# Performance work log

Measured on AMD Instinct MI355X. Metric: run time of the kernel, lower is better.

Reference implementation:

```python
import jax, jax.numpy as jnp
import numpy as np

B, T, N = 256, 512, 256
START, STOP = 254, 255


def setup_inputs() -> dict:
    key = jax.random.key(0)
    k1, k2, k3 = jax.random.split(key, 3)
    inputs = jax.random.normal(k1, (B, T, N), dtype=jnp.float32)
    transitions = jax.random.normal(k2, (N, N), dtype=jnp.float32)
    # sentinel rows/cols as in __init__
    transitions = transitions.at[START, :].set(-10000.0).at[:, STOP].set(-10000.0)
    tags = jax.random.randint(k3, (B, T), 0, N, dtype=jnp.int32)
    mask = jnp.ones((B, T), dtype=jnp.int32)
    return {"inputs": inputs, "transitions": transitions, "tags": tags, "mask": mask}


def _input_likelihood(inputs, transitions, fmask):
    # alpha[b, tag]: log-sum over paths ending at tag
    alpha0 = transitions[:, START][None, :] + inputs[:, 0, :]

    def step(alpha, xs):
        emit, m = xs  # emit: (B, N), m: (B,)
        # inner[b, next, prev] = alpha[b, prev] + (emit[b, next] + trans[next, prev]) * mask[b, i-1]
        inner = alpha[:, None, :] + (emit[:, :, None] + transitions[None, :, :]) * m[:, None, None]
        return jax.nn.logsumexp(inner, axis=-1), None

    xs = (jnp.swapaxes(inputs[:, 1:, :], 0, 1), jnp.swapaxes(fmask[:, :-1], 0, 1))
    alpha, _ = jax.lax.scan(step, alpha0, xs)
    stops = alpha + transitions[STOP][None, :]
    return jax.nn.logsumexp(stops, axis=-1)  # (B,)


def _joint_likelihood(inputs, transitions, tags, fmask):
    score = transitions[tags[:, 0], START]  # (B,)
    # transitions[next, prev] * mask[:, i+1], summed over steps
    trans_sc = transitions[tags[:, 1:], tags[:, :-1]] * fmask[:, 1:]
    # inputs[b, i, prev_tag] * mask[:, i]
    emit_sc = jnp.take_along_axis(inputs[:, :-1, :], tags[:, :-1, None], axis=2)[..., 0] * fmask[:, :-1]
    score = score + trans_sc.sum(axis=-1) + emit_sc.sum(axis=-1)
    last_idx = (fmask.sum(axis=-1) - 1.0).astype(jnp.int32)  # (B,)
    last_tags = jnp.take_along_axis(tags, last_idx[:, None], axis=1)[:, 0]
    last_input = jnp.take_along_axis(inputs[:, -1, :], last_tags[:, None], axis=1)[:, 0]
    return score + transitions[STOP, last_tags] + last_input * fmask[:, -1]


def reference(inputs, transitions, tags, mask):
    fmask = mask.astype(jnp.float32)
    log_denominator = _input_likelihood(inputs, transitions, fmask)
    log_numerator = _joint_likelihood(inputs, transitions, tags, fmask)
    return jnp.sum(log_numerator - log_denominator)
```

## Files before the change

kernel.cpp:

```cpp
#include <hip/hip_runtime.h>
#include <hip/hip_bf16.h>
#include <stdint.h>

#define B_    256
#define T_    512
#define N_    256
#define START_ 254
#define STOP_  255
#define GCOLS 16
#define NF    16
#define ND    32
#define LOG2E 1.4426950408889634f
#define LN2   0.6931471805599453f

#define WSB_OFF 65536
#define WCF_OFF 131072
#define WCB_OFF 131328

typedef __attribute__((ext_vector_type(4))) float floatx4;
typedef __attribute__((ext_vector_type(2))) long long llx2;
typedef __attribute__((ext_vector_type(4))) unsigned int uintx4;

__device__ __forceinline__ void lds_barrier() {
    asm volatile("s_waitcnt lgkmcnt(0)\n\ts_barrier" ::: "memory");
}

__device__ __forceinline__ int pk_fp8x4(float a, float b, float c, float d) {
    int r = __builtin_amdgcn_cvt_pk_fp8_f32(a, b, 0, false);
    return __builtin_amdgcn_cvt_pk_fp8_f32(c, d, r, true);
}
__device__ __forceinline__ int pk_bf8x4(float a, float b, float c, float d) {
    int r = __builtin_amdgcn_cvt_pk_bf8_f32(a, b, 0, false);
    return __builtin_amdgcn_cvt_pk_bf8_f32(c, d, r, true);
}
__device__ __forceinline__ long long mk64(int lo, int hi) {
    return ((long long)(unsigned long long)(unsigned)hi << 32) | (unsigned)lo;
}
__device__ __forceinline__ unsigned umax_(unsigned a, unsigned b) { return a > b ? a : b; }

struct DenomShared {
    alignas(16) char  V[2][4096];
    alignas(16) unsigned short mexp[GCOLS * 8];
    alignas(16) float sbuf[GCOLS * 20];
};

template<bool ISF>
__device__ __forceinline__ void denom_path(
    DenomShared& sh, const float* __restrict__ inputs,
    const float* __restrict__ trans, const int* __restrict__ mask,
    float* __restrict__ ws, int blkLocal)
{
    const int tid = threadIdx.x;
    const int w = tid >> 6;
    const int l = tid & 63;
    const int q = l >> 4;
    const int b = l & 15;
    const int bg = blkLocal * GCOLS + b;
    const int j0 = 32 * w + 4 * q;
    const int S = ISF ? 256 : 255;

    auto EIDX = [](int s) { return ISF ? s : (511 - s); };
    auto MIDX = [](int s) { return ISF ? (s - 1) : (511 - s); };

    const int wa0 = ((w >> 1) << 10) + ((q >> 1) << 8) + (b << 4)
                  + ((w & 1) << 3) + ((q & 1) << 2);
    const int rbase = l << 4;

    long long afrag[2][8];
    #pragma unroll
    for (int mt = 0; mt < 2; ++mt) {
        const int row = 32 * w + 16 * mt + b;
        #pragma unroll
        for (int kt = 0; kt < 8; ++kt) {
            float e[8];
            if (ISF) {
                const float* p = trans + row * N_ + kt * 32 + q * 8;
                floatx4 t0 = *(const floatx4*)p;
                floatx4 t1 = *(const floatx4*)(p + 4);
                #pragma unroll
                for (int jj = 0; jj < 4; ++jj) {
                    e[jj]     = __builtin_amdgcn_exp2f(t0[jj] * LOG2E);
                    e[jj + 4] = __builtin_amdgcn_exp2f(t1[jj] * LOG2E);
                }
            } else {
                #pragma unroll
                for (int jj = 0; jj < 8; ++jj) {
                    const int k = kt * 32 + q * 8 + jj;
                    e[jj] = __builtin_amdgcn_exp2f(trans[k * N_ + row] * LOG2E);
                }
            }
            afrag[mt][kt] = mk64(pk_fp8x4(e[0], e[1], e[2], e[3]),
                                 pk_fp8x4(e[4], e[5], e[6], e[7]));
        }
    }

    const float* emitp = inputs + (size_t)bg * T_ * N_;
    const int*   maskp = mask + bg * T_;
    float C = 0.f;
    float u[2][4];

    auto produce = [&]() {
        float mx = u[0][0], sm = 0.f;
        #pragma unroll
        for (int mt = 0; mt < 2; ++mt)
            #pragma unroll
            for (int r = 0; r < 4; ++r) { mx = fmaxf(mx, u[mt][r]); sm += u[mt][r]; }
        mx = fmaxf(mx, __shfl_xor(mx, 16, 64));
        mx = fmaxf(mx, __shfl_xor(mx, 32, 64));
        sm += __shfl_xor(sm, 32, 64);
        if (l < 16)
            sh.mexp[b * 8 + w] =
                (unsigned short)(__builtin_bit_cast(uint32_t, mx) >> 23);
        if (l < 32) sh.sbuf[b * 20 + w * 2 + q] = sm;
    };

    if (ISF) {
        #pragma unroll
        for (int mt = 0; mt < 2; ++mt) {
            floatx4 em = *(const floatx4*)(emitp + j0 + 16 * mt);
            #pragma unroll
            for (int r = 0; r < 4; ++r) {
                const int j = j0 + 16 * mt + r;
                u[mt][r] = __builtin_amdgcn_exp2f((trans[j * N_ + START_] + em[r]) * LOG2E);
            }
        }
    } else {
        #pragma unroll
        for (int mt = 0; mt < 2; ++mt) {
            floatx4 st = *(const floatx4*)(trans + STOP_ * N_ + j0 + 16 * mt);
            #pragma unroll
            for (int r = 0; r < 4; ++r)
                u[mt][r] = __builtin_amdgcn_exp2f(st[r] * LOG2E);
        }
    }
    {
        float xpi[2][4] = {{1.f,1.f,1.f,1.f},{1.f,1.f,1.f,1.f}};
        if (!ISF) {
            #pragma unroll
            for (int mt = 0; mt < 2; ++mt) {
                floatx4 e = *(const floatx4*)(emitp + (size_t)511 * N_ + j0 + 16 * mt);
                #pragma unroll
                for (int r = 0; r < 4; ++r)
                    xpi[mt][r] = __builtin_amdgcn_exp2f(e[r] * LOG2E);
            }
        }
        produce();
        #pragma unroll
        for (int mt = 0; mt < 2; ++mt)
            *(int*)(sh.V[0] + wa0 + (mt << 9)) =
                pk_bf8x4(u[mt][0] * xpi[mt][0], u[mt][1] * xpi[mt][1],
                         u[mt][2] * xpi[mt][2], u[mt][3] * xpi[mt][3]);
    }
    floatx4 ebuf[2][2];
    float   mrot[2];
    ebuf[0][0] = *(const floatx4*)(emitp + (size_t)EIDX(1) * N_ + j0);
    ebuf[0][1] = *(const floatx4*)(emitp + (size_t)EIDX(1) * N_ + j0 + 16);
    ebuf[1][0] = *(const floatx4*)(emitp + (size_t)EIDX(2) * N_ + j0);
    ebuf[1][1] = *(const floatx4*)(emitp + (size_t)EIDX(2) * N_ + j0 + 16);
    mrot[0] = (float)maskp[MIDX(1)];
    mrot[1] = (float)maskp[MIDX(2)];
    lds_barrier();

    auto body = [&](int s, int pr, int cur) {
        const int sp = (s + 2 <= S) ? s + 2 : S;
        floatx4 eC0 = *(const floatx4*)(emitp + (size_t)EIDX(sp) * N_ + j0);
        floatx4 eC1 = *(const floatx4*)(emitp + (size_t)EIDX(sp) * N_ + j0 + 16);
        const float mC = (float)maskp[MIDX(sp)];

        const char* vb = sh.V[pr];
        long long bf[8];
        #pragma unroll
        for (int p = 0; p < 4; ++p) {
            llx2 rd = *(const llx2*)(vb + (p << 10) + rbase);
            bf[2 * p]     = rd[0];
            bf[2 * p + 1] = rd[1];
        }

        uintx4 me = *(const uintx4*)&sh.mexp[b * 8];
        unsigned hi = umax_(umax_(me[0], me[1]), umax_(me[2], me[3]));
        unsigned lo = umax_(umax_(me[0] << 16, me[1] << 16),
                            umax_(me[2] << 16, me[3] << 16));
        const int eb = (int)(umax_(hi, lo) >> 16);
        const float rs = __builtin_bit_cast(float, (uint32_t)(249 - eb) << 23);
        const float dCf = (float)(122 - eb);

        float xpv[2][4];
        #pragma unroll
        for (int r = 0; r < 4; ++r) {
            if (ISF) {
                xpv[0][r] = __builtin_amdgcn_exp2f(fmaf(ebuf[cur][0][r], LOG2E, dCf));
                xpv[1][r] = __builtin_amdgcn_exp2f(fmaf(ebuf[cur][1][r], LOG2E, dCf));
            } else {
                xpv[0][r] = __builtin_amdgcn_exp2f(ebuf[cur][0][r] * LOG2E);
                xpv[1][r] = __builtin_amdgcn_exp2f(ebuf[cur][1][r] * LOG2E);
            }
        }

        floatx4 a0 = {0.f,0.f,0.f,0.f}, a1 = {0.f,0.f,0.f,0.f};
        floatx4 a2 = {0.f,0.f,0.f,0.f}, a3 = {0.f,0.f,0.f,0.f};
        #pragma unroll
        for (int kt = 0; kt < 4; ++kt) {
            a0 = __builtin_amdgcn_mfma_f32_16x16x32_fp8_bf8(afrag[0][kt],     bf[kt],     a0, 0, 0, 0);
            a1 = __builtin_amdgcn_mfma_f32_16x16x32_fp8_bf8(afrag[0][kt + 4], bf[kt + 4], a1, 0, 0, 0);
            a2 = __builtin_amdgcn_mfma_f32_16x16x32_fp8_bf8(afrag[1][kt],     bf[kt],     a2, 0, 0, 0);
            a3 = __builtin_amdgcn_mfma_f32_16x16x32_fp8_bf8(afrag[1][kt + 4], bf[kt + 4], a3, 0, 0, 0);
        }

        const bool live = (mrot[cur] != 0.f);
        float csv = 0.f;
        if (__any(!live)) {
            const float* sb = &sh.sbuf[b * 20];
            floatx4 s0 = *(const floatx4*)sb,       s1 = *(const floatx4*)(sb + 4);
            floatx4 s2 = *(const floatx4*)(sb + 8), s3 = *(const floatx4*)(sb + 12);
            csv = ((((s0[0] + s0[1]) + (s0[2] + s0[3])) +
                    ((s1[0] + s1[1]) + (s1[2] + s1[3]))) +
                   (((s2[0] + s2[1]) + (s2[2] + s2[3])) +
                    ((s3[0] + s3[1]) + (s3[2] + s3[3])))) * rs;
        }
        #pragma unroll
        for (int r = 0; r < 4; ++r) {
            const float v0 = a0[r] + a1[r], v1 = a2[r] + a3[r];
            if (ISF) {
                u[0][r] = live ? v0 * xpv[0][r] : csv;
                u[1][r] = live ? v1 * xpv[1][r] : csv;
            } else {
                u[0][r] = live ? v0 * rs : csv;
                u[1][r] = live ? v1 * rs : csv;
            }
        }
        C += (float)(eb - 122);

        produce();
        #pragma unroll
        for (int mt = 0; mt < 2; ++mt) {
            *(int*)(sh.V[pr ^ 1] + wa0 + (mt << 9)) = ISF
                ? pk_bf8x4(u[mt][0], u[mt][1], u[mt][2], u[mt][3])
                : pk_bf8x4(u[mt][0] * xpv[mt][0], u[mt][1] * xpv[mt][1],
                           u[mt][2] * xpv[mt][2], u[mt][3] * xpv[mt][3]);
        }
        lds_barrier();
        ebuf[cur][0] = eC0; ebuf[cur][1] = eC1;
        mrot[cur] = mC;
    };

    #pragma unroll 1
    for (int g = 0; g < 127; ++g) {
        body(2 * g + 1, 0, 0);
        body(2 * g + 2, 1, 1);
    }
    if (ISF) { body(255, 0, 0); body(256, 1, 1); }
    else     { body(255, 0, 0); }

    float* wsV = ws + (ISF ? 0 : WSB_OFF);
    #pragma unroll
    for (int mt = 0; mt < 2; ++mt) {
        floatx4 vv = {u[mt][0], u[mt][1], u[mt][2], u[mt][3]};
        *(floatx4*)&wsV[(size_t)bg * N_ + j0 + 16 * mt] = vv;
    }
    if (tid < 16) {
        float* wsC = ws + (ISF ? WCF_OFF : WCB_OFF);
        wsC[blkLocal * GCOLS + tid] = C;
    }
}

__global__ __launch_bounds__(512, 2) void crf_main(
    const float* __restrict__ inputs, const float* __restrict__ trans,
    const int* __restrict__ tags, const int* __restrict__ mask,
    float* __restrict__ out, float* __restrict__ ws)
{
    __shared__ DenomShared sh;

    if (blockIdx.x >= ND) {
        float* nred = sh.sbuf;
        int*   nredi = (int*)(sh.sbuf + 8);
        const int bb = blockIdx.x - ND;
        const int t  = threadIdx.x;
        const int tg = tags[bb * T_ + t];
        const float fm = (float)mask[bb * T_ + t];
        float part = 0.f;
        if (t >= 1)      part += trans[tg * N_ + tags[bb * T_ + t - 1]] * fm;
        if (t <= T_ - 2) part += inputs[((size_t)bb * T_ + t) * N_ + tg] * fm;
        int ms = mask[bb * T_ + t];
        #pragma unroll
        for (int off = 1; off < 64; off <<= 1) {
            part += __shfl_xor(part, off, 64);
            ms   += __shfl_xor(ms, off, 64);
        }
        if ((t & 63) == 0) { nred[t >> 6] = part; nredi[t >> 6] = ms; }
        __syncthreads();
        if (t == 0) {
            float tot = 0.f; int mtot = 0;
            for (int i = 0; i < 8; ++i) { tot += nred[i]; mtot += nredi[i]; }
            tot += trans[tags[bb * T_] * N_ + START_];
            const int last = mtot - 1;
            const int lt = tags[bb * T_ + last];
            tot += trans[STOP_ * N_ + lt]
                 + inputs[((size_t)bb * T_ + (T_ - 1)) * N_ + lt]
                   * (float)mask[bb * T_ + T_ - 1];
            atomicAdd(out, tot);
        }
        return;
    }

    if (blockIdx.x < NF) denom_path<true>(sh, inputs, trans, mask, ws, blockIdx.x);
    else                 denom_path<false>(sh, inputs, trans, mask, ws, blockIdx.x - NF);
}

__global__ __launch_bounds__(256) void crf_combine(
    const float* __restrict__ ws, float* __restrict__ out)
{
    __shared__ float red[4];
    const int bb = blockIdx.x;
    const int t = threadIdx.x;
    float p = ws[(size_t)bb * N_ + t] * ws[WSB_OFF + (size_t)bb * N_ + t];
    #pragma unroll
    for (int off = 1; off < 64; off <<= 1) p += __shfl_xor(p, off, 64);
    if ((t & 63) == 0) red[t >> 6] = p;
    __syncthreads();
    if (t == 0) {
        const float tot = red[0] + red[1] + red[2] + red[3];
        const float denom = (ws[WCF_OFF + bb] + ws[WCB_OFF + bb]
                             + __builtin_amdgcn_logf(tot)) * LN2;
        atomicAdd(out, -denom);
    }
}

extern "C" void kernel_launch(void* const* d_in, const int* in_sizes, int n_in,
                              void* d_out, int out_size, void* d_ws, size_t ws_size,
                              hipStream_t stream) {
    const float* inputs = (const float*)d_in[0];
    const float* trans  = (const float*)d_in[1];
    const int*   tags   = (const int*)d_in[2];
    const int*   mask   = (const int*)d_in[3];
    float* out = (float*)d_out;
    float* ws  = (float*)d_ws;
    hipMemsetAsync(out, 0, sizeof(float), stream);
    crf_main<<<dim3(ND + B_), dim3(512), 0, stream>>>(inputs, trans, tags, mask, out, ws);
    crf_combine<<<dim3(B_), dim3(256), 0, stream>>>(ws, out);
}
```

Measured before the change: 389.8 us.

## Use scaled 16x16x128 FP8 MFMA and add a mask-free fast path

Replaces the sixteen 16x16x32 fp8/bf8 MFMAs per step with four scaled 16x16x128 f8f6f4 MFMAs. The A fragments and the LDS layout of the B operand are reorganised to match. The per-step max exchange now stores float maxima per quarter-wave in LDS instead of shuffling and packing exponents. A block-wide mask scan picks a specialised loop that skips mask loads, the sum buffer and the dead-step handling when every mask entry is nonzero. The cost is an extra reduction of 32 LDS floats per step and a longer prologue.

```diff
diff --git a/kernel.cpp b/kernel.cpp
--- a/kernel.cpp
+++ b/kernel.cpp
@@ -18,8 +18,10 @@
 #define WCB_OFF 131328
 
 typedef __attribute__((ext_vector_type(4))) float floatx4;
-typedef __attribute__((ext_vector_type(2))) long long llx2;
 typedef __attribute__((ext_vector_type(4))) unsigned int uintx4;
+typedef __attribute__((ext_vector_type(8))) int v8i;
+
+template<bool X> struct BC { static constexpr bool value = X; };
 
 __device__ __forceinline__ void lds_barrier() {
     asm volatile("s_waitcnt lgkmcnt(0)\n\ts_barrier" ::: "memory");
@@ -33,15 +35,12 @@
     int r = __builtin_amdgcn_cvt_pk_bf8_f32(a, b, 0, false);
     return __builtin_amdgcn_cvt_pk_bf8_f32(c, d, r, true);
 }
-__device__ __forceinline__ long long mk64(int lo, int hi) {
-    return ((long long)(unsigned long long)(unsigned)hi << 32) | (unsigned)lo;
-}
-__device__ __forceinline__ unsigned umax_(unsigned a, unsigned b) { return a > b ? a : b; }
 
 struct DenomShared {
     alignas(16) char  V[2][4096];
-    alignas(16) unsigned short mexp[GCOLS * 8];
+    alignas(16) float mbuf[GCOLS * 36];
     alignas(16) float sbuf[GCOLS * 20];
+    int flag;
 };
 
 template<bool ISF>
@@ -58,62 +57,64 @@
     const int bg = blkLocal * GCOLS + b;
     const int j0 = 32 * w + 4 * q;
     const int S = ISF ? 256 : 255;
+    const int scl = 0x7F7F7F7F;
 
     auto EIDX = [](int s) { return ISF ? s : (511 - s); };
     auto MIDX = [](int s) { return ISF ? (s - 1) : (511 - s); };
 
-    const int wa0 = ((w >> 1) << 10) + ((q >> 1) << 8) + (b << 4)
-                  + ((w & 1) << 3) + ((q & 1) << 2);
+    int wa[2];
+    #pragma unroll
+    for (int mt = 0; mt < 2; ++mt)
+        wa[mt] = ((((2 * w + mt) >> 3) * 2 + mt) << 10)
+               + ((w & 3) << 8) + (b << 4) + (q << 2);
     const int rbase = l << 4;
 
-    long long afrag[2][8];
+    v8i afrag[2][2];
     #pragma unroll
     for (int mt = 0; mt < 2; ++mt) {
         const int row = 32 * w + 16 * mt + b;
         #pragma unroll
-        for (int kt = 0; kt < 8; ++kt) {
-            float e[8];
-            if (ISF) {
-                const float* p = trans + row * N_ + kt * 32 + q * 8;
-                floatx4 t0 = *(const floatx4*)p;
-                floatx4 t1 = *(const floatx4*)(p + 4);
-                #pragma unroll
-                for (int jj = 0; jj < 4; ++jj) {
-                    e[jj]     = __builtin_amdgcn_exp2f(t0[jj] * LOG2E);
-                    e[jj + 4] = __builtin_amdgcn_exp2f(t1[jj] * LOG2E);
-                }
-            } else {
-                #pragma unroll
-                for (int jj = 0; jj < 8; ++jj) {
-                    const int k = kt * 32 + q * 8 + jj;
-                    e[jj] = __builtin_amdgcn_exp2f(trans[k * N_ + row] * LOG2E);
-                }
-            }
-            afrag[mt][kt] = mk64(pk_fp8x4(e[0], e[1], e[2], e[3]),
-                                 pk_fp8x4(e[4], e[5], e[6], e[7]));
-        }
-    }
+        for (int c = 0; c < 2; ++c) {
+            v8i a;
+            #pragma unroll
+            for (int g8 = 0; g8 < 8; ++g8) {
+                float e[4];
+                if (ISF) {
+                    floatx4 t = *(const floatx4*)(trans + row * N_ + c * 128 + q * 32 + 4 * g8);
+                    #pragma unroll
+                    for (int ii = 0; ii < 4; ++ii)
+                        e[ii] = __builtin_amdgcn_exp2f(t[ii] * LOG2E);
+                } else {
+                    #pragma unroll
+                    for (int ii = 0; ii < 4; ++ii) {
+                        const int k = c * 128 + q * 32 + 4 * g8 + ii;
+                        e[ii] = __builtin_amdgcn_exp2f(trans[k * N_ + row] * LOG2E);
+                    }
+                }
+                a[g8] = pk_fp8x4(e[0], e[1], e[2], e[3]);
+            }
+            afrag[mt][c] = a;
+        }
+    }
+
+    {
+        const int* mrow = mask + blkLocal * GCOLS * T_;
+        bool hd = false;
+        #pragma unroll
+        for (int i = 0; i < GCOLS * T_ / 512; ++i)
+            hd |= (mrow[tid + 512 * i] == 0);
+        if (tid == 0) sh.flag = 0;
+        __syncthreads();
+        if (__any(hd) && l == 0) atomicOr(&sh.flag, 1);
+        __syncthreads();
+    }
+    const bool anyDead = (sh.flag != 0);
 
     const float* emitp = inputs + (size_t)bg * T_ * N_;
     const int*   maskp = mask + bg * T_;
     float C = 0.f;
     float u[2][4];
 
-    auto produce = [&]() {
-        float mx = u[0][0], sm = 0.f;
-        #pragma unroll
-        for (int mt = 0; mt < 2; ++mt)
-            #pragma unroll
-            for (int r = 0; r < 4; ++r) { mx = fmaxf(mx, u[mt][r]); sm += u[mt][r]; }
-        mx = fmaxf(mx, __shfl_xor(mx, 16, 64));
-        mx = fmaxf(mx, __shfl_xor(mx, 32, 64));
-        sm += __shfl_xor(sm, 32, 64);
-        if (l < 16)
-            sh.mexp[b * 8 + w] =
-                (unsigned short)(__builtin_bit_cast(uint32_t, mx) >> 23);
-        if (l < 32) sh.sbuf[b * 20 + w * 2 + q] = sm;
-    };
-
     if (ISF) {
         #pragma unroll
         for (int mt = 0; mt < 2; ++mt) {
@@ -134,6 +135,15 @@
         }
     }
     {
+        float mx = u[0][0], sm = 0.f;
+        #pragma unroll
+        for (int mt = 0; mt < 2; ++mt)
+            #pragma unroll
+            for (int r = 0; r < 4; ++r) { mx = fmaxf(mx, u[mt][r]); sm += u[mt][r]; }
+        sh.mbuf[b * 36 + w * 4 + q] = mx;
+        sm += __shfl_xor(sm, 32, 64);
+        if (l < 32) sh.sbuf[b * 20 + w * 2 + q] = sm;
+
         float xpi[2][4] = {{1.f,1.f,1.f,1.f},{1.f,1.f,1.f,1.f}};
         if (!ISF) {
             #pragma unroll
@@ -144,112 +154,156 @@
                     xpi[mt][r] = __builtin_amdgcn_exp2f(e[r] * LOG2E);
             }
         }
-        produce();
         #pragma unroll
         for (int mt = 0; mt < 2; ++mt)
-            *(int*)(sh.V[0] + wa0 + (mt << 9)) =
+            *(int*)(sh.V[0] + wa[mt]) =
                 pk_bf8x4(u[mt][0] * xpi[mt][0], u[mt][1] * xpi[mt][1],
                          u[mt][2] * xpi[mt][2], u[mt][3] * xpi[mt][3]);
     }
-    floatx4 ebuf[2][2];
-    float   mrot[2];
-    ebuf[0][0] = *(const floatx4*)(emitp + (size_t)EIDX(1) * N_ + j0);
-    ebuf[0][1] = *(const floatx4*)(emitp + (size_t)EIDX(1) * N_ + j0 + 16);
-    ebuf[1][0] = *(const floatx4*)(emitp + (size_t)EIDX(2) * N_ + j0);
-    ebuf[1][1] = *(const floatx4*)(emitp + (size_t)EIDX(2) * N_ + j0 + 16);
-    mrot[0] = (float)maskp[MIDX(1)];
-    mrot[1] = (float)maskp[MIDX(2)];
-    lds_barrier();
-
-    auto body = [&](int s, int pr, int cur) {
-        const int sp = (s + 2 <= S) ? s + 2 : S;
-        floatx4 eC0 = *(const floatx4*)(emitp + (size_t)EIDX(sp) * N_ + j0);
-        floatx4 eC1 = *(const floatx4*)(emitp + (size_t)EIDX(sp) * N_ + j0 + 16);
-        const float mC = (float)maskp[MIDX(sp)];
-
-        const char* vb = sh.V[pr];
-        long long bf[8];
-        #pragma unroll
-        for (int p = 0; p < 4; ++p) {
-            llx2 rd = *(const llx2*)(vb + (p << 10) + rbase);
-            bf[2 * p]     = rd[0];
-            bf[2 * p + 1] = rd[1];
-        }
-
-        uintx4 me = *(const uintx4*)&sh.mexp[b * 8];
-        unsigned hi = umax_(umax_(me[0], me[1]), umax_(me[2], me[3]));
-        unsigned lo = umax_(umax_(me[0] << 16, me[1] << 16),
-                            umax_(me[2] << 16, me[3] << 16));
-        const int eb = (int)(umax_(hi, lo) >> 16);
-        const float rs = __builtin_bit_cast(float, (uint32_t)(249 - eb) << 23);
-        const float dCf = (float)(122 - eb);
-
-        float xpv[2][4];
-        #pragma unroll
-        for (int r = 0; r < 4; ++r) {
-            if (ISF) {
-                xpv[0][r] = __builtin_amdgcn_exp2f(fmaf(ebuf[cur][0][r], LOG2E, dCf));
-                xpv[1][r] = __builtin_amdgcn_exp2f(fmaf(ebuf[cur][1][r], LOG2E, dCf));
+
+    auto run = [&](auto fastc) {
+        constexpr bool FAST = decltype(fastc)::value;
+        floatx4 ebuf[2][2];
+        float   mrot[2] = {1.f, 1.f};
+        ebuf[0][0] = *(const floatx4*)(emitp + (size_t)EIDX(1) * N_ + j0);
+        ebuf[0][1] = *(const floatx4*)(emitp + (size_t)EIDX(1) * N_ + j0 + 16);
+        ebuf[1][0] = *(const floatx4*)(emitp + (size_t)EIDX(2) * N_ + j0);
+        ebuf[1][1] = *(const floatx4*)(emitp + (size_t)EIDX(2) * N_ + j0 + 16);
+        if (!FAST) {
+            mrot[0] = (float)maskp[MIDX(1)];
+            mrot[1] = (float)maskp[MIDX(2)];
+        }
+        lds_barrier();
+
+        auto body = [&](int s, int pr, int cur) {
+            const int sp = (s + 2 <= S) ? s + 2 : S;
+            floatx4 eC0 = *(const floatx4*)(emitp + (size_t)EIDX(sp) * N_ + j0);
+            floatx4 eC1 = *(const floatx4*)(emitp + (size_t)EIDX(sp) * N_ + j0 + 16);
+            float mC = 1.f;
+            if (!FAST) mC = (float)maskp[MIDX(sp)];
+
+            const char* vb = sh.V[pr];
+            v8i bfrag[2];
+            #pragma unroll
+            for (int c = 0; c < 2; ++c) {
+                uintx4 r0 = *(const uintx4*)(vb + (c << 11) + rbase);
+                uintx4 r1 = *(const uintx4*)(vb + (c << 11) + 1024 + rbase);
+                v8i bf;
+                bf[0] = r0[0]; bf[1] = r0[1]; bf[2] = r0[2]; bf[3] = r0[3];
+                bf[4] = r1[0]; bf[5] = r1[1]; bf[6] = r1[2]; bf[7] = r1[3];
+                bfrag[c] = bf;
+            }
+
+            const float* mb = &sh.mbuf[b * 36];
+            float cmax;
+            {
+                floatx4 mm[8];
+                #pragma unroll
+                for (int i = 0; i < 8; ++i) mm[i] = *(const floatx4*)(mb + 4 * i);
+                floatx4 mv = mm[0];
+                #pragma unroll
+                for (int i = 1; i < 8; ++i)
+                    #pragma unroll
+                    for (int r = 0; r < 4; ++r) mv[r] = fmaxf(mv[r], mm[i][r]);
+                cmax = fmaxf(fmaxf(mv[0], mv[1]), fmaxf(mv[2], mv[3]));
+            }
+            const uint32_t cb = __builtin_bit_cast(uint32_t, cmax);
+            const int eb = (int)((cb >> 23) & 0xFFu);
+            const float rs = __builtin_bit_cast(float, (uint32_t)(249 - eb) << 23);
+            const float dCf = (float)(122 - eb);
+
+            float xpv[2][4];
+            #pragma unroll
+            for (int r = 0; r < 4; ++r) {
+                if (ISF) {
+                    xpv[0][r] = __builtin_amdgcn_exp2f(fmaf(ebuf[cur][0][r], LOG2E, dCf));
+                    xpv[1][r] = __builtin_amdgcn_exp2f(fmaf(ebuf[cur][1][r], LOG2E, dCf));
+                } else {
+                    xpv[0][r] = __builtin_amdgcn_exp2f(ebuf[cur][0][r] * LOG2E);
+                    xpv[1][r] = __builtin_amdgcn_exp2f(ebuf[cur][1][r] * LOG2E);
+                }
+            }
+
+            floatx4 a0 = {0.f,0.f,0.f,0.f}, a1 = {0.f,0.f,0.f,0.f};
+            a0 = __builtin_amdgcn_mfma_scale_f32_16x16x128_f8f6f4(
+                     afrag[0][0], bfrag[0], a0, 0, 1, 0, scl, 0, scl);
+            a1 = __builtin_amdgcn_mfma_scale_f32_16x16x128_f8f6f4(
+                     afrag[1][0], bfrag[0], a1, 0, 1, 0, scl, 0, scl);
+            a0 = __builtin_amdgcn_mfma_scale_f32_16x16x128_f8f6f4(
+                     afrag[0][1], bfrag[1], a0, 0, 1, 0, scl, 0, scl);
+            a1 = __builtin_amdgcn_mfma_scale_f32_16x16x128_f8f6f4(
+                     afrag[1][1], bfrag[1], a1, 0, 1, 0, scl, 0, scl);
+
+            if (FAST) {
+                #pragma unroll
+                for (int r = 0; r < 4; ++r) {
+                    if (ISF) {
+                        u[0][r] = a0[r] * xpv[0][r];
+                        u[1][r] = a1[r] * xpv[1][r];
+                    } else {
+                        u[0][r] = a0[r] * rs;
+                        u[1][r] = a1[r] * rs;
+                    }
+                }
             } else {
-                xpv[0][r] = __builtin_amdgcn_exp2f(ebuf[cur][0][r] * LOG2E);
-                xpv[1][r] = __builtin_amdgcn_exp2f(ebuf[cur][1][r] * LOG2E);
-            }
-        }
-
-        floatx4 a0 = {0.f,0.f,0.f,0.f}, a1 = {0.f,0.f,0.f,0.f};
-        floatx4 a2 = {0.f,0.f,0.f,0.f}, a3 = {0.f,0.f,0.f,0.f};
-        #pragma unroll
-        for (int kt = 0; kt < 4; ++kt) {
-            a0 = __builtin_amdgcn_mfma_f32_16x16x32_fp8_bf8(afrag[0][kt],     bf[kt],     a0, 0, 0, 0);
-            a1 = __builtin_amdgcn_mfma_f32_16x16x32_fp8_bf8(afrag[0][kt + 4], bf[kt + 4], a1, 0, 0, 0);
-            a2 = __builtin_amdgcn_mfma_f32_16x16x32_fp8_bf8(afrag[1][kt],     bf[kt],     a2, 0, 0, 0);
-            a3 = __builtin_amdgcn_mfma_f32_16x16x32_fp8_bf8(afrag[1][kt + 4], bf[kt + 4], a3, 0, 0, 0);
-        }
-
-        const bool live = (mrot[cur] != 0.f);
-        float csv = 0.f;
-        if (__any(!live)) {
-            const float* sb = &sh.sbuf[b * 20];
-            floatx4 s0 = *(const floatx4*)sb,       s1 = *(const floatx4*)(sb + 4);
-            floatx4 s2 = *(const floatx4*)(sb + 8), s3 = *(const floatx4*)(sb + 12);
-            csv = ((((s0[0] + s0[1]) + (s0[2] + s0[3])) +
-                    ((s1[0] + s1[1]) + (s1[2] + s1[3]))) +
-                   (((s2[0] + s2[1]) + (s2[2] + s2[3])) +
-                    ((s3[0] + s3[1]) + (s3[2] + s3[3])))) * rs;
-        }
-        #pragma unroll
-        for (int r = 0; r < 4; ++r) {
-            const float v0 = a0[r] + a1[r], v1 = a2[r] + a3[r];
-            if (ISF) {
-                u[0][r] = live ? v0 * xpv[0][r] : csv;
-                u[1][r] = live ? v1 * xpv[1][r] : csv;
-            } else {
-                u[0][r] = live ? v0 * rs : csv;
-                u[1][r] = live ? v1 * rs : csv;
-            }
-        }
-        C += (float)(eb - 122);
-
-        produce();
-        #pragma unroll
-        for (int mt = 0; mt < 2; ++mt) {
-            *(int*)(sh.V[pr ^ 1] + wa0 + (mt << 9)) = ISF
-                ? pk_bf8x4(u[mt][0], u[mt][1], u[mt][2], u[mt][3])
-                : pk_bf8x4(u[mt][0] * xpv[mt][0], u[mt][1] * xpv[mt][1],
-                           u[mt][2] * xpv[mt][2], u[mt][3] * xpv[mt][3]);
-        }
-        lds_barrier();
-        ebuf[cur][0] = eC0; ebuf[cur][1] = eC1;
-        mrot[cur] = mC;
+                const bool live = (mrot[cur] != 0.f);
+                float csv = 0.f;
+                if (__any(!live)) {
+                    const float* sb = &sh.sbuf[b * 20];
+                    floatx4 s0 = *(const floatx4*)sb,       s1 = *(const floatx4*)(sb + 4);
+                    floatx4 s2 = *(const floatx4*)(sb + 8), s3 = *(const floatx4*)(sb + 12);
+                    csv = ((((s0[0] + s0[1]) + (s0[2] + s0[3])) +
+                            ((s1[0] + s1[1]) + (s1[2] + s1[3]))) +
+                           (((s2[0] + s2[1]) + (s2[2] + s2[3])) +
+                            ((s3[0] + s3[1]) + (s3[2] + s3[3])))) * rs;
+                }
+                #pragma unroll
+                for (int r = 0; r < 4; ++r) {
+                    if (ISF) {
+                        u[0][r] = live ? a0[r] * xpv[0][r] : csv;
+                        u[1][r] = live ? a1[r] * xpv[1][r] : csv;
+                    } else {
+                        u[0][r] = live ? a0[r] * rs : csv;
+                        u[1][r] = live ? a1[r] * rs : csv;
+                    }
+                }
+            }
+            C += (float)(eb - 122);
+
+            {
+                float mx = fmaxf(fmaxf(fmaxf(u[0][0], u[0][1]), fmaxf(u[0][2], u[0][3])),
+                                 fmaxf(fmaxf(u[1][0], u[1][1]), fmaxf(u[1][2], u[1][3])));
+                sh.mbuf[b * 36 + w * 4 + q] = mx;
+                if (!FAST) {
+                    float sm = ((u[0][0] + u[0][1]) + (u[0][2] + u[0][3]))
+                             + ((u[1][0] + u[1][1]) + (u[1][2] + u[1][3]));
+                    sm += __shfl_xor(sm, 32, 64);
+                    if (l < 32) sh.sbuf[b * 20 + w * 2 + q] = sm;
+                }
+            }
+            #pragma unroll
+            for (int mt = 0; mt < 2; ++mt) {
+                *(int*)(sh.V[pr ^ 1] + wa[mt]) = ISF
+                    ? pk_bf8x4(u[mt][0], u[mt][1], u[mt][2], u[mt][3])
+                    : pk_bf8x4(u[mt][0] * xpv[mt][0], u[mt][1] * xpv[mt][1],
+                               u[mt][2] * xpv[mt][2], u[mt][3] * xpv[mt][3]);
+            }
+            lds_barrier();
+            ebuf[cur][0] = eC0; ebuf[cur][1] = eC1;
+            if (!FAST) mrot[cur] = mC;
+        };
+
+        #pragma unroll 1
+        for (int g = 0; g < 127; ++g) {
+            body(2 * g + 1, 0, 0);
+            body(2 * g + 2, 1, 1);
+        }
+        if (ISF) { body(255, 0, 0); body(256, 1, 1); }
+        else     { body(255, 0, 0); }
     };
 
-    #pragma unroll 1
-    for (int g = 0; g < 127; ++g) {
-        body(2 * g + 1, 0, 0);
-        body(2 * g + 2, 1, 1);
-    }
-    if (ISF) { body(255, 0, 0); body(256, 1, 1); }
-    else     { body(255, 0, 0); }
+    if (anyDead) run(BC<false>{});
+    else         run(BC<true>{});
 
     float* wsV = ws + (ISF ? 0 : WSB_OFF);
     #pragma unroll
```

New measurement: 344.0 us. 11.7% less time.
